# Kernel optimization log

Hardware: AMD Instinct MI355X
Metric: run time of the kernel (lower is better)

The kernel has to match this reference:

```python
import jax, jax.numpy as jnp
import numpy as np

R = 131072   # rays
S = 128      # existing samples per ray (existing_bins has S+1 edges)
N_NEW = 64   # new importance samples per ray
HIST_PAD = 1e-5   # NeuSSampler builds PDFSampler(histogram_padding=1e-5)
EPS = 1e-5


def setup_inputs() -> dict:
    key = jax.random.key(0)
    k1, k2, k3, k4 = jax.random.split(key, 4)
    weights = jax.random.uniform(k1, (R, S, 1), dtype=jnp.float32)
    # existing spacing bins must be sorted in [0,1] along the sample axis
    existing_bins = jnp.sort(jax.random.uniform(k2, (R, S + 1), dtype=jnp.float32), axis=-1)
    nears = 0.05 + 0.5 * jax.random.uniform(k3, (R, 1), dtype=jnp.float32)
    fars = nears + 1.0 + 3.0 * jax.random.uniform(k4, (R, 1), dtype=jnp.float32)
    return {"weights": weights, "existing_bins": existing_bins,
            "nears": nears, "fars": fars, "num_samples": N_NEW}


def reference(weights, existing_bins, nears, fars, num_samples):
    # PDFSampler.generate_ray_samples core (eval mode, include_original=False)
    num_bins = num_samples + 1
    w = weights[..., 0] + HIST_PAD                      # [R, S]
    w_sum = jnp.sum(w, axis=-1, keepdims=True)          # [R, 1]
    padding = jax.nn.relu(EPS - w_sum)
    w = w + padding / w.shape[-1]
    w_sum = w_sum + padding
    pdf = w / w_sum                                     # [R, S]
    cdf = jnp.minimum(jnp.ones_like(pdf), jnp.cumsum(pdf, axis=-1))
    cdf = jnp.concatenate([jnp.zeros_like(cdf[..., :1]), cdf], axis=-1)  # [R, S+1]

    # deterministic mid-bin query points (non-stratified branch)
    u = jnp.linspace(0.0, 1.0 - 1.0 / num_bins, num_bins, dtype=cdf.dtype)
    u = u + 1.0 / (2 * num_bins)
    u = jnp.broadcast_to(u, (*cdf.shape[:-1], num_bins))  # [R, num_bins]

    # inverse-CDF: per-ray binary search + gather + linear interp
    inds = jax.vmap(lambda c, q: jnp.searchsorted(c, q, side='right'))(cdf, u)
    last = existing_bins.shape[-1] - 1
    below = jnp.clip(inds - 1, 0, last)
    above = jnp.clip(inds, 0, last)
    cdf_g0 = jnp.take_along_axis(cdf, below, axis=-1)
    bins_g0 = jnp.take_along_axis(existing_bins, below, axis=-1)
    cdf_g1 = jnp.take_along_axis(cdf, above, axis=-1)
    bins_g1 = jnp.take_along_axis(existing_bins, above, axis=-1)
    t = jnp.clip(jnp.nan_to_num((u - cdf_g0) / (cdf_g1 - cdf_g0), nan=0.0,
                                posinf=0.0, neginf=0.0), 0.0, 1.0)
    bins = bins_g0 + t * (bins_g1 - bins_g0)            # [R, num_bins]
    bins = jax.lax.stop_gradient(bins)                  # torch: bins.detach()

    # spacing_to_euclidean_fn for UniformSampler: x*s_far + (1-x)*s_near
    euclidean_bins = bins * fars + (1.0 - bins) * nears  # [R, num_bins]
    return euclidean_bins
```

## Files before the change

kernel.cpp:

```cpp
#include <hip/hip_runtime.h>


#define DPP_FADD(x, ctrl, rmask)                                             \
    ((x) + __int_as_float(__builtin_amdgcn_update_dpp(                       \
               0, __float_as_int(x), (ctrl), (rmask), 0xf, true)))

#define DPP_UMAX(x, ctrl, rmask)                                             \
    (umax_((x), (unsigned)__builtin_amdgcn_update_dpp(                       \
               0, (int)(x), (ctrl), (rmask), 0xf, true)))

__device__ __forceinline__ unsigned umax_(unsigned a, unsigned b) {
    return a > b ? a : b;
}

__global__ __launch_bounds__(256) void neus_sampler_kernel(
    const float* __restrict__ weights,
    const float* __restrict__ bins_g,
    const float* __restrict__ nears,
    const float* __restrict__ fars,
    float* __restrict__ out,
    int R)
{
    constexpr int S  = 128;
    constexpr int NB = 65;
    constexpr float HPAD = 1e-5f;

    __shared__ float4   pay[4][S];
    __shared__ unsigned best[4][66];

    const int lane = threadIdx.x & 63;
    const int wv   = threadIdx.x >> 6;
    const int ray  = blockIdx.x * 4 + wv;
    if (ray >= R) return;
    const int uray = __builtin_amdgcn_readfirstlane(ray);

    if (lane < 33)
        *reinterpret_cast<unsigned long long*>(&best[wv][2 * lane]) = 0ull;

    const float2 wpair =
        reinterpret_cast<const float2*>(weights + (size_t)uray * S)[lane];
    const float* brow = bins_g + (size_t)uray * (S + 1);
    const float2 bpair = reinterpret_cast<const float2*>(brow)[lane];
    const float b_last = brow[S];

    const float w1 = wpair.y + HPAD;
    float ps = (wpair.x + HPAD) + w1;

    ps = DPP_FADD(ps, 0x111, 0xf);
    ps = DPP_FADD(ps, 0x112, 0xf);
    ps = DPP_FADD(ps, 0x114, 0xf);
    ps = DPP_FADD(ps, 0x118, 0xf);
    ps = DPP_FADD(ps, 0x142, 0xa);
    ps = DPP_FADD(ps, 0x143, 0xc);

    const float total =
        __int_as_float(__builtin_amdgcn_readlane(__float_as_int(ps), 63));
    const float padding = fmaxf(1e-5f - total, 0.0f);
    const float padc    = padding * (1.0f / S);
    const float inv     = __builtin_amdgcn_rcpf(total + padding);

    const float c_hi  = fminf(1.0f, fmaf((float)(2 * lane + 2), padc, ps) * inv);
    const float c_mid = fminf(1.0f, fmaf((float)(2 * lane + 1), padc, ps - w1) * inv);
    float c_lo = __shfl_up(c_hi, 1, 64);
    if (lane == 0) c_lo = 0.0f;
    float b2 = __shfl_down(bpair.x, 1, 64);
    if (lane == 63) b2 = b_last;

    const float nearv = nears[uray];
    const float farv  = fars[uray];
    const float fmn   = farv - nearv;

    pay[wv][2 * lane] = make_float4(
        c_lo, c_mid - c_lo, fmaf(bpair.x, fmn, nearv), (bpair.y - bpair.x) * fmn);
    pay[wv][2 * lane + 1] = make_float4(
        c_mid, c_hi - c_mid, fmaf(bpair.y, fmn, nearv), (b2 - bpair.y) * fmn);

    auto jf = [](float c) -> int {
        int j = (int)ceilf(fmaf(65.0f, c, -0.5f));
        return j < 0 ? 0 : (j > NB ? NB : j);
    };

    atomicMax(&best[wv][jf(c_lo)],  (unsigned)(2 * lane));
    atomicMax(&best[wv][jf(c_mid)], (unsigned)(2 * lane + 1));

    asm volatile("s_waitcnt lgkmcnt(0)" ::: "memory");

    unsigned m = best[wv][lane];
    m = DPP_UMAX(m, 0x111, 0xf);
    m = DPP_UMAX(m, 0x112, 0xf);
    m = DPP_UMAX(m, 0x114, 0xf);
    m = DPP_UMAX(m, 0x118, 0xf);
    m = DPP_UMAX(m, 0x142, 0xa);
    m = DPP_UMAX(m, 0x143, 0xc);

    float* const orow = out + (size_t)uray * NB;
    {
        const float4 p  = pay[wv][m];
        const float  u  = (float)(2 * lane + 1) * (1.0f / 130.0f);
        const float  t  = (u - p.x) * __builtin_amdgcn_rcpf(p.y);
        const float  tc = fminf(fmaxf(t, 0.0f), 1.0f);
        orow[lane] = fmaf(tc, p.w, p.z);
    }
    if (lane == 63) {
        const unsigned m64 = umax_(m, best[wv][64]);
        const float4 p  = pay[wv][m64];
        const float  t  = (129.0f / 130.0f - p.x) * __builtin_amdgcn_rcpf(p.y);
        const float  tc = fminf(fmaxf(t, 0.0f), 1.0f);
        orow[64] = fmaf(tc, p.w, p.z);
    }
}

extern "C" void kernel_launch(void* const* d_in, const int* in_sizes, int n_in,
                              void* d_out, int out_size, void* d_ws, size_t ws_size,
                              hipStream_t stream) {
    const float* weights = (const float*)d_in[0];
    const float* ebins   = (const float*)d_in[1];
    const float* nears   = (const float*)d_in[2];
    const float* fars    = (const float*)d_in[3];
    float* out = (float*)d_out;
    const int R = in_sizes[0] / 128;
    const int blocks = (R + 3) / 4;
    hipLaunchKernelGGL(neus_sampler_kernel, dim3(blocks), dim3(256), 0, stream,
                       weights, ebins, nears, fars, out, R);
}
```

Baseline: 162.5 us.

## Use persistent grid-stride waves with next-ray prefetch and SoA shared payload

Caps the grid at 2048 blocks and turns each wave into a persistent loop over rays, loading the next ray's weights, bins and near/far values into registers while the current ray is processed. This is meant to hide global load latency and cut block launch overhead. The shared payload also moves from float4 AoS to four SoA float arrays, and only lane 63 loads the last bin edge. The risks are more register pressure and the loss of a missing barrier between iterations: the `best` array is re-zeroed at the top of each iteration with only an lgkmcnt wait protecting it.

```diff
diff --git a/kernel.cpp b/kernel.cpp
--- a/kernel.cpp
+++ b/kernel.cpp
@@ -5,12 +5,36 @@
     ((x) + __int_as_float(__builtin_amdgcn_update_dpp(                       \
                0, __float_as_int(x), (ctrl), (rmask), 0xf, true)))
 
+__device__ __forceinline__ unsigned umax_(unsigned a, unsigned b) {
+    return a > b ? a : b;
+}
+
 #define DPP_UMAX(x, ctrl, rmask)                                             \
     (umax_((x), (unsigned)__builtin_amdgcn_update_dpp(                       \
                0, (int)(x), (ctrl), (rmask), 0xf, true)))
 
-__device__ __forceinline__ unsigned umax_(unsigned a, unsigned b) {
-    return a > b ? a : b;
+struct RayIn {
+    float2 wpair;
+    float2 bpair;
+    float  bl;
+    float  nearv;
+    float  farv;
+};
+
+__device__ __forceinline__ RayIn load_ray(const float* __restrict__ weights,
+                                          const float* __restrict__ bins_g,
+                                          const float* __restrict__ nears,
+                                          const float* __restrict__ fars,
+                                          int uray, int lane)
+{
+    RayIn r;
+    r.wpair = reinterpret_cast<const float2*>(weights + (size_t)uray * 128)[lane];
+    const float* brow = bins_g + (size_t)uray * 129;
+    r.bpair = reinterpret_cast<const float2*>(brow)[lane];
+    r.bl    = (lane == 63) ? brow[128] : 0.0f;
+    r.nearv = nears[uray];
+    r.farv  = fars[uray];
+    return r;
 }
 
 __global__ __launch_bounds__(256) void neus_sampler_kernel(
@@ -21,92 +45,112 @@
     float* __restrict__ out,
     int R)
 {
-    constexpr int S  = 128;
     constexpr int NB = 65;
     constexpr float HPAD = 1e-5f;
 
-    __shared__ float4   pay[4][S];
+    __shared__ float    payc[4][128];
+    __shared__ float    payd[4][128];
+    __shared__ float    payb[4][128];
+    __shared__ float    pays[4][128];
     __shared__ unsigned best[4][66];
 
     const int lane = threadIdx.x & 63;
     const int wv   = threadIdx.x >> 6;
-    const int ray  = blockIdx.x * 4 + wv;
-    if (ray >= R) return;
-    const int uray = __builtin_amdgcn_readfirstlane(ray);
-
-    if (lane < 33)
-        *reinterpret_cast<unsigned long long*>(&best[wv][2 * lane]) = 0ull;
-
-    const float2 wpair =
-        reinterpret_cast<const float2*>(weights + (size_t)uray * S)[lane];
-    const float* brow = bins_g + (size_t)uray * (S + 1);
-    const float2 bpair = reinterpret_cast<const float2*>(brow)[lane];
-    const float b_last = brow[S];
-
-    const float w1 = wpair.y + HPAD;
-    float ps = (wpair.x + HPAD) + w1;
-
-    ps = DPP_FADD(ps, 0x111, 0xf);
-    ps = DPP_FADD(ps, 0x112, 0xf);
-    ps = DPP_FADD(ps, 0x114, 0xf);
-    ps = DPP_FADD(ps, 0x118, 0xf);
-    ps = DPP_FADD(ps, 0x142, 0xa);
-    ps = DPP_FADD(ps, 0x143, 0xc);
-
-    const float total =
-        __int_as_float(__builtin_amdgcn_readlane(__float_as_int(ps), 63));
-    const float padding = fmaxf(1e-5f - total, 0.0f);
-    const float padc    = padding * (1.0f / S);
-    const float inv     = __builtin_amdgcn_rcpf(total + padding);
-
-    const float c_hi  = fminf(1.0f, fmaf((float)(2 * lane + 2), padc, ps) * inv);
-    const float c_mid = fminf(1.0f, fmaf((float)(2 * lane + 1), padc, ps - w1) * inv);
-    float c_lo = __shfl_up(c_hi, 1, 64);
-    if (lane == 0) c_lo = 0.0f;
-    float b2 = __shfl_down(bpair.x, 1, 64);
-    if (lane == 63) b2 = b_last;
-
-    const float nearv = nears[uray];
-    const float farv  = fars[uray];
-    const float fmn   = farv - nearv;
-
-    pay[wv][2 * lane] = make_float4(
-        c_lo, c_mid - c_lo, fmaf(bpair.x, fmn, nearv), (bpair.y - bpair.x) * fmn);
-    pay[wv][2 * lane + 1] = make_float4(
-        c_mid, c_hi - c_mid, fmaf(bpair.y, fmn, nearv), (b2 - bpair.y) * fmn);
+    const int gw   = blockIdx.x * 4 + wv;
+    const int stride = gridDim.x * 4;
+    if (gw >= R) return;
 
     auto jf = [](float c) -> int {
         int j = (int)ceilf(fmaf(65.0f, c, -0.5f));
         return j < 0 ? 0 : (j > NB ? NB : j);
     };
 
-    atomicMax(&best[wv][jf(c_lo)],  (unsigned)(2 * lane));
-    atomicMax(&best[wv][jf(c_mid)], (unsigned)(2 * lane + 1));
+    int ray = gw;
+    RayIn cur = load_ray(weights, bins_g, nears, fars,
+                         __builtin_amdgcn_readfirstlane(ray), lane);
 
-    asm volatile("s_waitcnt lgkmcnt(0)" ::: "memory");
+    while (true) {
+        const int nray = ray + stride;
+        const bool have = (nray < R);
+        RayIn nxt;
+        if (have)
+            nxt = load_ray(weights, bins_g, nears, fars,
+                           __builtin_amdgcn_readfirstlane(nray), lane);
 
-    unsigned m = best[wv][lane];
-    m = DPP_UMAX(m, 0x111, 0xf);
-    m = DPP_UMAX(m, 0x112, 0xf);
-    m = DPP_UMAX(m, 0x114, 0xf);
-    m = DPP_UMAX(m, 0x118, 0xf);
-    m = DPP_UMAX(m, 0x142, 0xa);
-    m = DPP_UMAX(m, 0x143, 0xc);
+        const int uray = __builtin_amdgcn_readfirstlane(ray);
 
-    float* const orow = out + (size_t)uray * NB;
-    {
-        const float4 p  = pay[wv][m];
-        const float  u  = (float)(2 * lane + 1) * (1.0f / 130.0f);
-        const float  t  = (u - p.x) * __builtin_amdgcn_rcpf(p.y);
-        const float  tc = fminf(fmaxf(t, 0.0f), 1.0f);
-        orow[lane] = fmaf(tc, p.w, p.z);
-    }
-    if (lane == 63) {
-        const unsigned m64 = umax_(m, best[wv][64]);
-        const float4 p  = pay[wv][m64];
-        const float  t  = (129.0f / 130.0f - p.x) * __builtin_amdgcn_rcpf(p.y);
-        const float  tc = fminf(fmaxf(t, 0.0f), 1.0f);
-        orow[64] = fmaf(tc, p.w, p.z);
+        if (lane < 33)
+            *reinterpret_cast<unsigned long long*>(&best[wv][2 * lane]) = 0ull;
+
+        const float w1 = cur.wpair.y + HPAD;
+        float ps = (cur.wpair.x + HPAD) + w1;
+
+        ps = DPP_FADD(ps, 0x111, 0xf);
+        ps = DPP_FADD(ps, 0x112, 0xf);
+        ps = DPP_FADD(ps, 0x114, 0xf);
+        ps = DPP_FADD(ps, 0x118, 0xf);
+        ps = DPP_FADD(ps, 0x142, 0xa);
+        ps = DPP_FADD(ps, 0x143, 0xc);
+
+        const float total =
+            __int_as_float(__builtin_amdgcn_readlane(__float_as_int(ps), 63));
+        const float padding = fmaxf(1e-5f - total, 0.0f);
+        const float padc    = padding * (1.0f / 128.0f);
+        const float inv     = __builtin_amdgcn_rcpf(total + padding);
+
+        const float c_hi  = fminf(1.0f, fmaf((float)(2 * lane + 2), padc, ps) * inv);
+        const float c_mid = fminf(1.0f, fmaf((float)(2 * lane + 1), padc, ps - w1) * inv);
+        float c_lo = __shfl_up(c_hi, 1, 64);
+        if (lane == 0) c_lo = 0.0f;
+        float b2 = __shfl_down(cur.bpair.x, 1, 64);
+        if (lane == 63) b2 = cur.bl;
+
+        const float nearv = cur.nearv;
+        const float fmn   = cur.farv - nearv;
+
+        payc[wv][2 * lane]     = c_lo;
+        payc[wv][2 * lane + 1] = c_mid;
+        payd[wv][2 * lane]     = c_mid - c_lo;
+        payd[wv][2 * lane + 1] = c_hi - c_mid;
+        payb[wv][2 * lane]     = fmaf(cur.bpair.x, fmn, nearv);
+        payb[wv][2 * lane + 1] = fmaf(cur.bpair.y, fmn, nearv);
+        pays[wv][2 * lane]     = (cur.bpair.y - cur.bpair.x) * fmn;
+        pays[wv][2 * lane + 1] = (b2 - cur.bpair.y) * fmn;
+
+        atomicMax(&best[wv][jf(c_lo)],  (unsigned)(2 * lane));
+        atomicMax(&best[wv][jf(c_mid)], (unsigned)(2 * lane + 1));
+
+        asm volatile("s_waitcnt lgkmcnt(0)" ::: "memory");
+
+        unsigned m = best[wv][lane];
+        m = DPP_UMAX(m, 0x111, 0xf);
+        m = DPP_UMAX(m, 0x112, 0xf);
+        m = DPP_UMAX(m, 0x114, 0xf);
+        m = DPP_UMAX(m, 0x118, 0xf);
+        m = DPP_UMAX(m, 0x142, 0xa);
+        m = DPP_UMAX(m, 0x143, 0xc);
+
+        float* const orow = out + (size_t)uray * NB;
+        {
+            const float px = payc[wv][m], py = payd[wv][m];
+            const float pz = payb[wv][m], pw = pays[wv][m];
+            const float u  = (float)(2 * lane + 1) * (1.0f / 130.0f);
+            const float t  = (u - px) * __builtin_amdgcn_rcpf(py);
+            const float tc = fminf(fmaxf(t, 0.0f), 1.0f);
+            orow[lane] = fmaf(tc, pw, pz);
+        }
+        if (lane == 63) {
+            const unsigned m64 = umax_(m, best[wv][64]);
+            const float px = payc[wv][m64], py = payd[wv][m64];
+            const float pz = payb[wv][m64], pw = pays[wv][m64];
+            const float t  = (129.0f / 130.0f - px) * __builtin_amdgcn_rcpf(py);
+            const float tc = fminf(fmaxf(t, 0.0f), 1.0f);
+            orow[64] = fmaf(tc, pw, pz);
+        }
+
+        if (!have) break;
+        cur = nxt;
+        ray = nray;
     }
 }
 
@@ -119,7 +163,8 @@
     const float* fars    = (const float*)d_in[3];
     float* out = (float*)d_out;
     const int R = in_sizes[0] / 128;
-    const int blocks = (R + 3) / 4;
+    int blocks = (R + 3) / 4;
+    if (blocks > 2048) blocks = 2048;
     hipLaunchKernelGGL(neus_sampler_kernel, dim3(blocks), dim3(256), 0, stream,
                        weights, ebins, nears, fars, out, R);
 }
```

Result: slower. 167.8 us (+3.3%).

## Use persistent blocks with double-buffered global_load_lds staging of ray rows

Applied to the files above, without the earlier changes.

The kernel becomes a persistent-grid kernel capped at 2048 blocks. Each block walks a contiguous range of 8-ray chunks and prefetches the next chunk's weights and bins into LDS with async global_load_lds, double-buffered and synchronised with vmcnt waits and barriers. Each wave now handles two rays per iteration, and the float4 payload is split into four scalar LDS arrays. The goal is to hide global memory latency and cut launch and occupancy overhead, at the cost of more LDS use, extra barriers, and a fallback path for tail chunks.

```diff
diff --git a/kernel.cpp b/kernel.cpp
--- a/kernel.cpp
+++ b/kernel.cpp
@@ -5,13 +5,26 @@
     ((x) + __int_as_float(__builtin_amdgcn_update_dpp(                       \
                0, __float_as_int(x), (ctrl), (rmask), 0xf, true)))
 
+__device__ __forceinline__ unsigned umax_(unsigned a, unsigned b) {
+    return a > b ? a : b;
+}
 #define DPP_UMAX(x, ctrl, rmask)                                             \
     (umax_((x), (unsigned)__builtin_amdgcn_update_dpp(                       \
                0, (int)(x), (ctrl), (rmask), 0xf, true)))
 
-__device__ __forceinline__ unsigned umax_(unsigned a, unsigned b) {
-    return a > b ? a : b;
-}
+__device__ __forceinline__ void gll16(const float* g, float* l) {
+    __builtin_amdgcn_global_load_lds(
+        (const __attribute__((address_space(1))) void*)g,
+        (__attribute__((address_space(3))) void*)l, 16, 0, 0);
+}
+
+#define WAITV(n) asm volatile("s_waitcnt vmcnt(" #n ")" ::: "memory")
+#define BARRIER()                                                            \
+    do {                                                                     \
+        asm volatile("" ::: "memory");                                       \
+        __builtin_amdgcn_s_barrier();                                        \
+        asm volatile("" ::: "memory");                                       \
+    } while (0)
 
 __global__ __launch_bounds__(256) void neus_sampler_kernel(
     const float* __restrict__ weights,
@@ -21,92 +34,162 @@
     float* __restrict__ out,
     int R)
 {
-    constexpr int S  = 128;
-    constexpr int NB = 65;
+    constexpr int NB  = 65;
+    constexpr int RPB = 8;
     constexpr float HPAD = 1e-5f;
 
-    __shared__ float4   pay[4][S];
-    __shared__ unsigned best[4][66];
+    __shared__ alignas(16) float Wl[2][RPB * 128];
+    __shared__ alignas(16) float Bl[2][RPB * 129];
+    __shared__ float payc[4][2][128];
+    __shared__ float payd[4][2][128];
+    __shared__ float payb[4][2][128];
+    __shared__ float pays[4][2][128];
+    __shared__ alignas(8) unsigned best[4][2][66];
 
     const int lane = threadIdx.x & 63;
     const int wv   = threadIdx.x >> 6;
-    const int ray  = blockIdx.x * 4 + wv;
-    if (ray >= R) return;
-    const int uray = __builtin_amdgcn_readfirstlane(ray);
-
-    if (lane < 33)
-        *reinterpret_cast<unsigned long long*>(&best[wv][2 * lane]) = 0ull;
-
-    const float2 wpair =
-        reinterpret_cast<const float2*>(weights + (size_t)uray * S)[lane];
-    const float* brow = bins_g + (size_t)uray * (S + 1);
-    const float2 bpair = reinterpret_cast<const float2*>(brow)[lane];
-    const float b_last = brow[S];
-
-    const float w1 = wpair.y + HPAD;
-    float ps = (wpair.x + HPAD) + w1;
-
-    ps = DPP_FADD(ps, 0x111, 0xf);
-    ps = DPP_FADD(ps, 0x112, 0xf);
-    ps = DPP_FADD(ps, 0x114, 0xf);
-    ps = DPP_FADD(ps, 0x118, 0xf);
-    ps = DPP_FADD(ps, 0x142, 0xa);
-    ps = DPP_FADD(ps, 0x143, 0xc);
-
-    const float total =
-        __int_as_float(__builtin_amdgcn_readlane(__float_as_int(ps), 63));
-    const float padding = fmaxf(1e-5f - total, 0.0f);
-    const float padc    = padding * (1.0f / S);
-    const float inv     = __builtin_amdgcn_rcpf(total + padding);
-
-    const float c_hi  = fminf(1.0f, fmaf((float)(2 * lane + 2), padc, ps) * inv);
-    const float c_mid = fminf(1.0f, fmaf((float)(2 * lane + 1), padc, ps - w1) * inv);
-    float c_lo = __shfl_up(c_hi, 1, 64);
-    if (lane == 0) c_lo = 0.0f;
-    float b2 = __shfl_down(bpair.x, 1, 64);
-    if (lane == 63) b2 = b_last;
-
-    const float nearv = nears[uray];
-    const float farv  = fars[uray];
-    const float fmn   = farv - nearv;
-
-    pay[wv][2 * lane] = make_float4(
-        c_lo, c_mid - c_lo, fmaf(bpair.x, fmn, nearv), (bpair.y - bpair.x) * fmn);
-    pay[wv][2 * lane + 1] = make_float4(
-        c_mid, c_hi - c_mid, fmaf(bpair.y, fmn, nearv), (b2 - bpair.y) * fmn);
+
+    const int NBt   = (R + RPB - 1) / RPB;
+    const int K     = (NBt + (int)gridDim.x - 1) / (int)gridDim.x;
+    const int b0    = (int)blockIdx.x * K;
+    const int bEnd  = (b0 + K < NBt) ? b0 + K : NBt;
+    if (b0 >= bEnd) return;
+    const int NFULL = R / RPB;
 
     auto jf = [](float c) -> int {
         int j = (int)ceilf(fmaf(65.0f, c, -0.5f));
         return j < 0 ? 0 : (j > NB ? NB : j);
     };
 
-    atomicMax(&best[wv][jf(c_lo)],  (unsigned)(2 * lane));
-    atomicMax(&best[wv][jf(c_mid)], (unsigned)(2 * lane + 1));
-
-    asm volatile("s_waitcnt lgkmcnt(0)" ::: "memory");
-
-    unsigned m = best[wv][lane];
-    m = DPP_UMAX(m, 0x111, 0xf);
-    m = DPP_UMAX(m, 0x112, 0xf);
-    m = DPP_UMAX(m, 0x114, 0xf);
-    m = DPP_UMAX(m, 0x118, 0xf);
-    m = DPP_UMAX(m, 0x142, 0xa);
-    m = DPP_UMAX(m, 0x143, 0xc);
-
-    float* const orow = out + (size_t)uray * NB;
-    {
-        const float4 p  = pay[wv][m];
-        const float  u  = (float)(2 * lane + 1) * (1.0f / 130.0f);
-        const float  t  = (u - p.x) * __builtin_amdgcn_rcpf(p.y);
-        const float  tc = fminf(fmaxf(t, 0.0f), 1.0f);
-        orow[lane] = fmaf(tc, p.w, p.z);
-    }
-    if (lane == 63) {
-        const unsigned m64 = umax_(m, best[wv][64]);
-        const float4 p  = pay[wv][m64];
-        const float  t  = (129.0f / 130.0f - p.x) * __builtin_amdgcn_rcpf(p.y);
-        const float  tc = fminf(fmaxf(t, 0.0f), 1.0f);
-        orow[64] = fmaf(tc, p.w, p.z);
+    auto stage = [&](int b, int buf) {
+        const float* gw = weights + (size_t)b * (RPB * 128) + wv * 256 + lane * 4;
+        gll16(gw, &Wl[buf][wv * 256]);
+        const float* gb = bins_g + (size_t)b * (RPB * 129) + wv * 256 + lane * 4;
+        gll16(gb, &Bl[buf][wv * 256]);
+        if (wv == 3)
+            gll16(bins_g + (size_t)b * (RPB * 129) + 776 + lane * 4,
+                  &Bl[buf][776]);
+    };
+
+    auto doPhase1 = [&](float2 wpair, float2 bpair, float bl,
+                        float nearv, float farv, int slot) {
+        if (lane < 33)
+            *reinterpret_cast<unsigned long long*>(&best[wv][slot][2 * lane]) = 0ull;
+
+        const float w1 = wpair.y + HPAD;
+        float ps = (wpair.x + HPAD) + w1;
+        ps = DPP_FADD(ps, 0x111, 0xf);
+        ps = DPP_FADD(ps, 0x112, 0xf);
+        ps = DPP_FADD(ps, 0x114, 0xf);
+        ps = DPP_FADD(ps, 0x118, 0xf);
+        ps = DPP_FADD(ps, 0x142, 0xa);
+        ps = DPP_FADD(ps, 0x143, 0xc);
+
+        const float total =
+            __int_as_float(__builtin_amdgcn_readlane(__float_as_int(ps), 63));
+        const float padding = fmaxf(1e-5f - total, 0.0f);
+        const float padc    = padding * (1.0f / 128.0f);
+        const float inv     = __builtin_amdgcn_rcpf(total + padding);
+
+        const float c_hi  = fminf(1.0f, fmaf((float)(2 * lane + 2), padc, ps) * inv);
+        const float c_mid = fminf(1.0f, fmaf((float)(2 * lane + 1), padc, ps - w1) * inv);
+        float c_lo = __shfl_up(c_hi, 1, 64);
+        if (lane == 0) c_lo = 0.0f;
+        float b2 = __shfl_down(bpair.x, 1, 64);
+        if (lane == 63) b2 = bl;
+
+        const float fmn = farv - nearv;
+        payc[wv][slot][2 * lane]     = c_lo;
+        payc[wv][slot][2 * lane + 1] = c_mid;
+        payd[wv][slot][2 * lane]     = c_mid - c_lo;
+        payd[wv][slot][2 * lane + 1] = c_hi - c_mid;
+        payb[wv][slot][2 * lane]     = fmaf(bpair.x, fmn, nearv);
+        payb[wv][slot][2 * lane + 1] = fmaf(bpair.y, fmn, nearv);
+        pays[wv][slot][2 * lane]     = (bpair.y - bpair.x) * fmn;
+        pays[wv][slot][2 * lane + 1] = (b2 - bpair.y) * fmn;
+
+        atomicMax(&best[wv][slot][jf(c_lo)],  (unsigned)(2 * lane));
+        atomicMax(&best[wv][slot][jf(c_mid)], (unsigned)(2 * lane + 1));
+    };
+
+    auto doPhase2 = [&](int uray, int slot) {
+        unsigned m = best[wv][slot][lane];
+        m = DPP_UMAX(m, 0x111, 0xf);
+        m = DPP_UMAX(m, 0x112, 0xf);
+        m = DPP_UMAX(m, 0x114, 0xf);
+        m = DPP_UMAX(m, 0x118, 0xf);
+        m = DPP_UMAX(m, 0x142, 0xa);
+        m = DPP_UMAX(m, 0x143, 0xc);
+
+        float* const orow = out + (size_t)uray * NB;
+        const float px = payc[wv][slot][m], py = payd[wv][slot][m];
+        const float pz = payb[wv][slot][m], pw = pays[wv][slot][m];
+        const float u  = (float)(2 * lane + 1) * (1.0f / 130.0f);
+        const float t  = (u - px) * __builtin_amdgcn_rcpf(py);
+        const float tc = fminf(fmaxf(t, 0.0f), 1.0f);
+        orow[lane] = fmaf(tc, pw, pz);
+        if (lane == 63) {
+            const unsigned m64 = umax_(m, best[wv][slot][64]);
+            const float qx = payc[wv][slot][m64], qy = payd[wv][slot][m64];
+            const float qz = payb[wv][slot][m64], qw = pays[wv][slot][m64];
+            const float t2  = (129.0f / 130.0f - qx) * __builtin_amdgcn_rcpf(qy);
+            const float tc2 = fminf(fmaxf(t2, 0.0f), 1.0f);
+            orow[64] = fmaf(tc2, qw, qz);
+        }
+    };
+
+    int buf = 0;
+    if (b0 < NFULL) stage(b0, 0);
+
+    for (int b = b0; b < bEnd; ++b) {
+        const int nb = b + 1;
+        const bool donext = (nb < bEnd) && (nb < NFULL);
+        if (donext) stage(nb, buf ^ 1);
+
+        if (b < NFULL) {
+            if (!donext)      WAITV(0);
+            else if (wv == 3) WAITV(3);
+            else              WAITV(2);
+            BARRIER();
+
+            const int urA  = __builtin_amdgcn_readfirstlane(b * RPB + wv);
+            const int urB  = urA + 4;
+            const int rowA = wv, rowB = wv + 4;
+
+            const float2 wA = *reinterpret_cast<const float2*>(
+                &Wl[buf][rowA * 128 + 2 * lane]);
+            const float bA0 = Bl[buf][rowA * 129 + 2 * lane];
+            const float bA1 = Bl[buf][rowA * 129 + 2 * lane + 1];
+            const float blA = Bl[buf][rowA * 129 + 128];
+            const float2 wB = *reinterpret_cast<const float2*>(
+                &Wl[buf][rowB * 128 + 2 * lane]);
+            const float bB0 = Bl[buf][rowB * 129 + 2 * lane];
+            const float bB1 = Bl[buf][rowB * 129 + 2 * lane + 1];
+            const float blB = Bl[buf][rowB * 129 + 128];
+
+            doPhase1(wA, make_float2(bA0, bA1), blA, nears[urA], fars[urA], 0);
+            doPhase1(wB, make_float2(bB0, bB1), blB, nears[urB], fars[urB], 1);
+            asm volatile("s_waitcnt lgkmcnt(0)" ::: "memory");
+            doPhase2(urA, 0);
+            doPhase2(urB, 1);
+
+            BARRIER();
+        } else {
+            for (int k = 0; k < 2; ++k) {
+                const int rr = b * RPB + wv + 4 * k;
+                if (rr < R) {
+                    const int ur = __builtin_amdgcn_readfirstlane(rr);
+                    const float2 wp = reinterpret_cast<const float2*>(
+                        weights + (size_t)ur * 128)[lane];
+                    const float* brow = bins_g + (size_t)ur * 129;
+                    const float2 bp = reinterpret_cast<const float2*>(brow)[lane];
+                    doPhase1(wp, bp, brow[128], nears[ur], fars[ur], k);
+                    asm volatile("s_waitcnt lgkmcnt(0)" ::: "memory");
+                    doPhase2(ur, k);
+                }
+            }
+        }
+        buf ^= 1;
     }
 }
 
@@ -119,7 +202,8 @@
     const float* fars    = (const float*)d_in[3];
     float* out = (float*)d_out;
     const int R = in_sizes[0] / 128;
-    const int blocks = (R + 3) / 4;
+    const int NBt = (R + 7) / 8;
+    int blocks = NBt < 2048 ? NBt : 2048;
     hipLaunchKernelGGL(neus_sampler_kernel, dim3(blocks), dim3(256), 0, stream,
                        weights, ebins, nears, fars, out, R);
 }
```

After: 175.5 us. 1.08x slower.

## Process two rays per wavefront and split LDS payload into SoA arrays

Applied to the files above, without the earlier changes.

Each wavefront now handles two consecutive rays, issuing all global loads for both rays up front and running both prefix-sum/scatter phases before a single LDS wait. This aims to raise memory-level parallelism and amortize per-wave overhead and launch size. The float4 payload is also split into four separate float arrays, which turns the gather into four scalar LDS reads instead of one vector read. The costs are more registers and LDS per wave, and half as many waves launched.

```diff
diff --git a/kernel.cpp b/kernel.cpp
--- a/kernel.cpp
+++ b/kernel.cpp
@@ -5,13 +5,12 @@
     ((x) + __int_as_float(__builtin_amdgcn_update_dpp(                       \
                0, __float_as_int(x), (ctrl), (rmask), 0xf, true)))
 
+__device__ __forceinline__ unsigned umax_(unsigned a, unsigned b) {
+    return a > b ? a : b;
+}
 #define DPP_UMAX(x, ctrl, rmask)                                             \
     (umax_((x), (unsigned)__builtin_amdgcn_update_dpp(                       \
                0, (int)(x), (ctrl), (rmask), 0xf, true)))
-
-__device__ __forceinline__ unsigned umax_(unsigned a, unsigned b) {
-    return a > b ? a : b;
-}
 
 __global__ __launch_bounds__(256) void neus_sampler_kernel(
     const float* __restrict__ weights,
@@ -21,93 +20,113 @@
     float* __restrict__ out,
     int R)
 {
-    constexpr int S  = 128;
     constexpr int NB = 65;
     constexpr float HPAD = 1e-5f;
 
-    __shared__ float4   pay[4][S];
-    __shared__ unsigned best[4][66];
+    __shared__ float payc[4][2][128];
+    __shared__ float payd[4][2][128];
+    __shared__ float payb[4][2][128];
+    __shared__ float pays[4][2][128];
+    __shared__ alignas(8) unsigned best[4][2][66];
 
     const int lane = threadIdx.x & 63;
     const int wv   = threadIdx.x >> 6;
-    const int ray  = blockIdx.x * 4 + wv;
-    if (ray >= R) return;
-    const int uray = __builtin_amdgcn_readfirstlane(ray);
+    const int gw   = blockIdx.x * 4 + wv;
+    const int rayA = gw * 2;
+    if (rayA >= R) return;
+    const int urA   = __builtin_amdgcn_readfirstlane(rayA);
+    const bool haveB = (rayA + 1 < R);
+    const int urB   = haveB ? urA + 1 : urA;
 
-    if (lane < 33)
-        *reinterpret_cast<unsigned long long*>(&best[wv][2 * lane]) = 0ull;
-
-    const float2 wpair =
-        reinterpret_cast<const float2*>(weights + (size_t)uray * S)[lane];
-    const float* brow = bins_g + (size_t)uray * (S + 1);
-    const float2 bpair = reinterpret_cast<const float2*>(brow)[lane];
-    const float b_last = brow[S];
-
-    const float w1 = wpair.y + HPAD;
-    float ps = (wpair.x + HPAD) + w1;
-
-    ps = DPP_FADD(ps, 0x111, 0xf);
-    ps = DPP_FADD(ps, 0x112, 0xf);
-    ps = DPP_FADD(ps, 0x114, 0xf);
-    ps = DPP_FADD(ps, 0x118, 0xf);
-    ps = DPP_FADD(ps, 0x142, 0xa);
-    ps = DPP_FADD(ps, 0x143, 0xc);
-
-    const float total =
-        __int_as_float(__builtin_amdgcn_readlane(__float_as_int(ps), 63));
-    const float padding = fmaxf(1e-5f - total, 0.0f);
-    const float padc    = padding * (1.0f / S);
-    const float inv     = __builtin_amdgcn_rcpf(total + padding);
-
-    const float c_hi  = fminf(1.0f, fmaf((float)(2 * lane + 2), padc, ps) * inv);
-    const float c_mid = fminf(1.0f, fmaf((float)(2 * lane + 1), padc, ps - w1) * inv);
-    float c_lo = __shfl_up(c_hi, 1, 64);
-    if (lane == 0) c_lo = 0.0f;
-    float b2 = __shfl_down(bpair.x, 1, 64);
-    if (lane == 63) b2 = b_last;
-
-    const float nearv = nears[uray];
-    const float farv  = fars[uray];
-    const float fmn   = farv - nearv;
-
-    pay[wv][2 * lane] = make_float4(
-        c_lo, c_mid - c_lo, fmaf(bpair.x, fmn, nearv), (bpair.y - bpair.x) * fmn);
-    pay[wv][2 * lane + 1] = make_float4(
-        c_mid, c_hi - c_mid, fmaf(bpair.y, fmn, nearv), (b2 - bpair.y) * fmn);
+    const float2 wA = reinterpret_cast<const float2*>(weights + (size_t)urA * 128)[lane];
+    const float* browA = bins_g + (size_t)urA * 129;
+    const float2 bA = reinterpret_cast<const float2*>(browA)[lane];
+    const float2 wB = reinterpret_cast<const float2*>(weights + (size_t)urB * 128)[lane];
+    const float* browB = bins_g + (size_t)urB * 129;
+    const float2 bB = reinterpret_cast<const float2*>(browB)[lane];
+    const float blA = browA[128], blB = browB[128];
+    const float nA = nears[urA], fA = fars[urA];
+    const float nB = nears[urB], fB = fars[urB];
 
     auto jf = [](float c) -> int {
         int j = (int)ceilf(fmaf(65.0f, c, -0.5f));
         return j < 0 ? 0 : (j > NB ? NB : j);
     };
 
-    atomicMax(&best[wv][jf(c_lo)],  (unsigned)(2 * lane));
-    atomicMax(&best[wv][jf(c_mid)], (unsigned)(2 * lane + 1));
+    auto doPhase1 = [&](float2 wpair, float2 bpair, float bl,
+                        float nearv, float farv, int slot) {
+        if (lane < 33)
+            *reinterpret_cast<unsigned long long*>(&best[wv][slot][2 * lane]) = 0ull;
+
+        const float w1 = wpair.y + HPAD;
+        float ps = (wpair.x + HPAD) + w1;
+        ps = DPP_FADD(ps, 0x111, 0xf);
+        ps = DPP_FADD(ps, 0x112, 0xf);
+        ps = DPP_FADD(ps, 0x114, 0xf);
+        ps = DPP_FADD(ps, 0x118, 0xf);
+        ps = DPP_FADD(ps, 0x142, 0xa);
+        ps = DPP_FADD(ps, 0x143, 0xc);
+
+        const float total =
+            __int_as_float(__builtin_amdgcn_readlane(__float_as_int(ps), 63));
+        const float padding = fmaxf(1e-5f - total, 0.0f);
+        const float padc    = padding * (1.0f / 128.0f);
+        const float inv     = __builtin_amdgcn_rcpf(total + padding);
+
+        const float c_hi  = fminf(1.0f, fmaf((float)(2 * lane + 2), padc, ps) * inv);
+        const float c_mid = fminf(1.0f, fmaf((float)(2 * lane + 1), padc, ps - w1) * inv);
+        float c_lo = __shfl_up(c_hi, 1, 64);
+        if (lane == 0) c_lo = 0.0f;
+        float b2 = __shfl_down(bpair.x, 1, 64);
+        if (lane == 63) b2 = bl;
+
+        const float fmn = farv - nearv;
+        payc[wv][slot][2 * lane]     = c_lo;
+        payc[wv][slot][2 * lane + 1] = c_mid;
+        payd[wv][slot][2 * lane]     = c_mid - c_lo;
+        payd[wv][slot][2 * lane + 1] = c_hi - c_mid;
+        payb[wv][slot][2 * lane]     = fmaf(bpair.x, fmn, nearv);
+        payb[wv][slot][2 * lane + 1] = fmaf(bpair.y, fmn, nearv);
+        pays[wv][slot][2 * lane]     = (bpair.y - bpair.x) * fmn;
+        pays[wv][slot][2 * lane + 1] = (b2 - bpair.y) * fmn;
+
+        atomicMax(&best[wv][slot][jf(c_lo)],  (unsigned)(2 * lane));
+        atomicMax(&best[wv][slot][jf(c_mid)], (unsigned)(2 * lane + 1));
+    };
+
+    auto doPhase2 = [&](int uray, int slot) {
+        unsigned m = best[wv][slot][lane];
+        m = DPP_UMAX(m, 0x111, 0xf);
+        m = DPP_UMAX(m, 0x112, 0xf);
+        m = DPP_UMAX(m, 0x114, 0xf);
+        m = DPP_UMAX(m, 0x118, 0xf);
+        m = DPP_UMAX(m, 0x142, 0xa);
+        m = DPP_UMAX(m, 0x143, 0xc);
+
+        float* const orow = out + (size_t)uray * NB;
+        const float px = payc[wv][slot][m], py = payd[wv][slot][m];
+        const float pz = payb[wv][slot][m], pw = pays[wv][slot][m];
+        const float u  = (float)(2 * lane + 1) * (1.0f / 130.0f);
+        const float t  = (u - px) * __builtin_amdgcn_rcpf(py);
+        const float tc = fminf(fmaxf(t, 0.0f), 1.0f);
+        orow[lane] = fmaf(tc, pw, pz);
+        if (lane == 63) {
+            const unsigned m64 = umax_(m, best[wv][slot][64]);
+            const float qx = payc[wv][slot][m64], qy = payd[wv][slot][m64];
+            const float qz = payb[wv][slot][m64], qw = pays[wv][slot][m64];
+            const float t2  = (129.0f / 130.0f - qx) * __builtin_amdgcn_rcpf(qy);
+            const float tc2 = fminf(fmaxf(t2, 0.0f), 1.0f);
+            orow[64] = fmaf(tc2, qw, qz);
+        }
+    };
+
+    doPhase1(wA, bA, blA, nA, fA, 0);
+    doPhase1(wB, bB, blB, nB, fB, 1);
 
     asm volatile("s_waitcnt lgkmcnt(0)" ::: "memory");
 
-    unsigned m = best[wv][lane];
-    m = DPP_UMAX(m, 0x111, 0xf);
-    m = DPP_UMAX(m, 0x112, 0xf);
-    m = DPP_UMAX(m, 0x114, 0xf);
-    m = DPP_UMAX(m, 0x118, 0xf);
-    m = DPP_UMAX(m, 0x142, 0xa);
-    m = DPP_UMAX(m, 0x143, 0xc);
-
-    float* const orow = out + (size_t)uray * NB;
-    {
-        const float4 p  = pay[wv][m];
-        const float  u  = (float)(2 * lane + 1) * (1.0f / 130.0f);
-        const float  t  = (u - p.x) * __builtin_amdgcn_rcpf(p.y);
-        const float  tc = fminf(fmaxf(t, 0.0f), 1.0f);
-        orow[lane] = fmaf(tc, p.w, p.z);
-    }
-    if (lane == 63) {
-        const unsigned m64 = umax_(m, best[wv][64]);
-        const float4 p  = pay[wv][m64];
-        const float  t  = (129.0f / 130.0f - p.x) * __builtin_amdgcn_rcpf(p.y);
-        const float  tc = fminf(fmaxf(t, 0.0f), 1.0f);
-        orow[64] = fmaf(tc, p.w, p.z);
-    }
+    doPhase2(urA, 0);
+    if (haveB) doPhase2(urB, 1);
 }
 
 extern "C" void kernel_launch(void* const* d_in, const int* in_sizes, int n_in,
@@ -119,7 +138,8 @@
     const float* fars    = (const float*)d_in[3];
     float* out = (float*)d_out;
     const int R = in_sizes[0] / 128;
-    const int blocks = (R + 3) / 4;
+    const int waves = (R + 1) / 2;
+    const int blocks = (waves + 3) / 4;
     hipLaunchKernelGGL(neus_sampler_kernel, dim3(blocks), dim3(256), 0, stream,
                        weights, ebins, nears, fars, out, R);
 }
```

Measured after the change: 163.8 us. No clear change (+0.8%).
